# Kernel tuning notes

Measured on AMD Instinct MI355X. Metric: run time of the kernel, lower is better.

## Reference

```python
import jax, jax.numpy as jnp
import numpy as np
import math

N_HEADS = 16
STRIDE = 4
LN_EPS = 1e-5
ROPE_BASE = 10000.0


def rotate_half(x):
    h = x.shape[-1] // 2
    return jnp.concatenate([-x[..., h:], x[..., :h]], axis=-1)


def rope_cos_sin(seq_len, head_dim, dtype):
    inv_freq = 1.0 / (ROPE_BASE ** (jnp.arange(0, head_dim, 2, dtype=jnp.float32) / head_dim))
    t = jnp.arange(seq_len, dtype=jnp.float32)
    freqs = jnp.outer(t, inv_freq)                      # [S, hd/2]
    emb = jnp.concatenate([freqs, freqs], axis=-1)      # [S, hd]
    return jnp.cos(emb).astype(dtype), jnp.sin(emb).astype(dtype)


def linear_upsample(x, T):
    # x: [B, Ts, D] -> [B, T, D]; matches F.interpolate(mode='linear', align_corners=False)
    Ts = x.shape[1]
    scale = Ts / T
    src = (jnp.arange(T, dtype=jnp.float32) + 0.5) * scale - 0.5
    src = jnp.clip(src, 0.0, Ts - 1.0)
    i0 = jnp.floor(src).astype(jnp.int32)
    i1 = jnp.minimum(i0 + 1, Ts - 1)
    w = (src - i0.astype(jnp.float32)).astype(x.dtype)[None, :, None]
    return x[:, i0, :] * (1.0 - w) + x[:, i1, :] * w


def setup_inputs() -> dict:
    key = jax.random.key(0)
    ks = jax.random.split(key, 4)
    B, T, D = 4, 4096, 1024
    s = 1.0 / math.sqrt(D)
    return {
        "x": jax.random.normal(ks[0], (B, T, D), dtype=jnp.float32),
        "norm_w": jnp.ones((D,), dtype=jnp.float32),
        "norm_b": jnp.zeros((D,), dtype=jnp.float32),
        "W_qkv": jax.random.normal(ks[1], (D, 3 * D), dtype=jnp.float32) * s,
        "b_qkv": jnp.zeros((3 * D,), dtype=jnp.float32),
        "W_out": jax.random.normal(ks[2], (D, D), dtype=jnp.float32) * s,
        "b_out": jnp.zeros((D,), dtype=jnp.float32),
    }


def reference(x, norm_w, norm_b, W_qkv, b_qkv, W_out, b_out):
    B, T, D = x.shape
    H = N_HEADS
    hd = D // H
    residual = x

    # LayerNorm (biased variance, eps=1e-5)
    mu = jnp.mean(x, axis=-1, keepdims=True)
    var = jnp.var(x, axis=-1, keepdims=True)
    x_norm = (x - mu) * jax.lax.rsqrt(var + LN_EPS) * norm_w + norm_b

    # strided downsample (T >= 2*stride path)
    xs = x_norm[:, ::STRIDE, :]
    Ts = xs.shape[1]

    # fused QKV projection
    qkv = xs @ W_qkv + b_qkv                             # [B, Ts, 3D]
    qkv = qkv.reshape(B, Ts, 3, H, hd).transpose(2, 0, 3, 1, 4)
    q, k, v = qkv[0], qkv[1], qkv[2]                     # [B, H, Ts, hd]

    # RoPE
    cos, sin = rope_cos_sin(Ts, hd, q.dtype)             # [Ts, hd]
    q = q * cos + rotate_half(q) * sin
    k = k * cos + rotate_half(k) * sin

    # causal SDPA on strided subsequence
    scores = jnp.einsum('bhqd,bhkd->bhqk', q, k) / math.sqrt(hd)
    causal = jnp.tril(jnp.ones((Ts, Ts), dtype=bool))
    scores = jnp.where(causal, scores, jnp.finfo(scores.dtype).min)
    attn = jax.nn.softmax(scores, axis=-1)
    out = jnp.einsum('bhqk,bhkd->bhqd', attn, v)         # [B, H, Ts, hd]
    out = out.transpose(0, 2, 1, 3).reshape(B, Ts, D)

    out = out @ W_out + b_out
    out = linear_upsample(out, T)                        # [B, T, D]
    return residual + out
```

## Files before the change

kernel.cpp:

```cpp
#include <hip/hip_runtime.h>
#include <hip/hip_bf16.h>

#define DEVFN __device__ __forceinline__

typedef float f32x4 __attribute__((ext_vector_type(4)));
typedef float f32x16 __attribute__((ext_vector_type(16)));
typedef __bf16 bf16x8 __attribute__((ext_vector_type(8)));
typedef unsigned short u16x8 __attribute__((ext_vector_type(8)));
typedef unsigned short u16x4 __attribute__((ext_vector_type(4)));
typedef unsigned u32x4 __attribute__((ext_vector_type(4)));

DEVFN unsigned short f2bf(float f) {
  unsigned u = __builtin_bit_cast(unsigned, f);
  u = (u + 0x7FFFu + ((u >> 16) & 1u)) >> 16;
  return (unsigned short)u;
}

DEVFN f32x4 mfma_bf16(u16x8 a, u16x8 b, f32x4 c) {
  return __builtin_amdgcn_mfma_f32_16x16x32_bf16((bf16x8)a, (bf16x8)b, c, 0, 0, 0);
}

DEVFN f32x16 mfma32(u16x8 a, u16x8 b, f32x16 c) {
  return __builtin_amdgcn_mfma_f32_32x32x16_bf16((bf16x8)a, (bf16x8)b, c, 0, 0, 0);
}

DEVFN unsigned cvt_pk_bf16(float a, float b) {
  unsigned r;
  asm("v_cvt_pk_bf16_f32 %0, %1, %2" : "=v"(r) : "v"(a), "v"(b));
  return r;
}

DEVFN void permswap(unsigned& a, unsigned& b) {
  asm("v_permlane32_swap_b32 %0, %1" : "+v"(a), "+v"(b));
}

DEVFN void sincos_rev(float rev, float* sn, float* cs) {
  float fr, s, c;
  asm("v_fract_f32 %0, %1" : "=v"(fr) : "v"(rev));
  asm("v_sin_f32 %0, %1" : "=v"(s) : "v"(fr));
  asm("v_cos_f32 %0, %1" : "=v"(c) : "v"(fr));
  *sn = s; *cs = c;
}

DEVFN void gload_lds16(const void* g, void* l) {
  __builtin_amdgcn_global_load_lds(
      (const __attribute__((address_space(1))) void*)g,
      (__attribute__((address_space(3))) void*)l, 16, 0, 0);
}

__global__ __launch_bounds__(256) void ln_stride_kernel(
    const float* __restrict__ x, const float* __restrict__ w,
    const float* __restrict__ bb, unsigned short* __restrict__ xs,
    int T, int Ts, int D, int stride) {
  int row = blockIdx.x;
  int b = row / Ts, ts = row - b * Ts;
  const float* xr = x + ((size_t)b * T + (size_t)ts * stride) * D;
  int t = threadIdx.x;
  float4 v = *(const float4*)(xr + t * 4);
  float s = v.x + v.y + v.z + v.w;
  float sq = v.x * v.x + v.y * v.y + v.z * v.z + v.w * v.w;
#pragma unroll
  for (int m = 1; m < 64; m <<= 1) { s += __shfl_xor(s, m); sq += __shfl_xor(sq, m); }
  __shared__ float ps[4], pq[4];
  if ((t & 63) == 0) { ps[t >> 6] = s; pq[t >> 6] = sq; }
  __syncthreads();
  s = ps[0] + ps[1] + ps[2] + ps[3];
  sq = pq[0] + pq[1] + pq[2] + pq[3];
  float invD = 1.0f / (float)D;
  float mu = s * invD;
  float var = sq * invD - mu * mu;
  float rs = rsqrtf(var + 1e-5f);
  int c = t * 4;
  float4 wv = *(const float4*)(w + c);
  float4 bv = *(const float4*)(bb + c);
  u16x4 o;
  o[0] = f2bf((v.x - mu) * rs * wv.x + bv.x);
  o[1] = f2bf((v.y - mu) * rs * wv.y + bv.y);
  o[2] = f2bf((v.z - mu) * rs * wv.z + bv.z);
  o[3] = f2bf((v.w - mu) * rs * wv.w + bv.w);
  *(u16x4*)(xs + (size_t)row * D + c) = o;
}

__global__ __launch_bounds__(256) void wconv_kernel(
    const float* __restrict__ W, unsigned short* __restrict__ Wt, int K, int N) {
  __shared__ float tile[32][33];
  int n0 = blockIdx.x * 32, k0 = blockIdx.y * 32;
  int tx = threadIdx.x & 31, ty = threadIdx.x >> 5;
#pragma unroll
  for (int i = 0; i < 32; i += 8) tile[ty + i][tx] = W[(size_t)(k0 + ty + i) * N + n0 + tx];
  __syncthreads();
#pragma unroll
  for (int i = 0; i < 32; i += 8) Wt[(size_t)(n0 + ty + i) * K + k0 + tx] = f2bf(tile[tx][ty + i]);
}

__global__ __launch_bounds__(512, 1) void gemm_qkv256_kernel(
    const unsigned short* __restrict__ A, const unsigned short* __restrict__ Bt,
    const float* __restrict__ bias, int M, int N, int Kd,
    unsigned short* __restrict__ Qo, unsigned short* __restrict__ Ko,
    unsigned short* __restrict__ Vt) {
  __shared__ __align__(128) char lds[131072];
  const int tid = threadIdx.x, l = tid & 63, w = tid >> 6;
  const int wr = w >> 2, wc = w & 3;
  const int lg = l >> 4, lr = l & 15;
  const int o = blockIdx.x;
  const int xcd = o & 7, s = o >> 3;
  const int bm = (xcd & 3) * 4 + (s & 3);
  const int bn = (xcd >> 2) * 6 + (s >> 2);
  const int m0 = bm << 8, n0 = bn << 8;
  const int chk = (lg ^ ((lr >> 1) & 3)) << 4;

  f32x4 acc[8][4] = {};

#define STAGE32(kk, bufoff)                                                 \
  do {                                                                      \
    _Pragma("unroll")                                                       \
    for (int i_ = 0; i_ < 2; i_++) {                                        \
      int c_ = tid + (i_ << 9);                                             \
      int rl_ = c_ >> 2, c4_ = c_ & 3;                                      \
      int cs_ = c4_ ^ ((rl_ >> 1) & 3);                                     \
      gload_lds16(A + (size_t)(m0 + rl_) * Kd + (kk) + cs_ * 8,             \
                  lds + (bufoff) + c_ * 16);                                \
      gload_lds16(Bt + (size_t)(n0 + rl_) * Kd + (kk) + cs_ * 8,            \
                  lds + (bufoff) + 16384 + c_ * 16);                        \
    }                                                                       \
  } while (0)

  STAGE32(0, 0);
  STAGE32(32, 32768);
  STAGE32(64, 65536);

  const int NT = Kd >> 5;
  for (int t = 0; t < NT; ++t) {
    if (t < NT - 2)       asm volatile("s_waitcnt vmcnt(8)" ::: "memory");
    else if (t == NT - 2) asm volatile("s_waitcnt vmcnt(4)" ::: "memory");
    else                  asm volatile("s_waitcnt vmcnt(0)" ::: "memory");
    __builtin_amdgcn_s_barrier();
    const int curoff = (t & 3) << 15;

    u16x8 bfr[4], afr[8];
#pragma unroll
    for (int nf = 0; nf < 4; nf++)
      bfr[nf] = *(const u16x8*)(lds + curoff + 16384 +
                                (wc * 64 + nf * 16 + lr) * 64 + chk);
#pragma unroll
    for (int mf = 0; mf < 8; mf++)
      afr[mf] = *(const u16x8*)(lds + curoff +
                                (wr * 128 + mf * 16 + lr) * 64 + chk);
    if (t + 3 < NT) STAGE32((t + 3) << 5, ((t + 3) & 3) << 15);
    asm volatile("s_waitcnt lgkmcnt(0)" ::: "memory");
    __builtin_amdgcn_sched_barrier(0);
    __builtin_amdgcn_s_setprio(1);
#pragma unroll
    for (int mf = 0; mf < 8; mf++)
#pragma unroll
      for (int nf = 0; nf < 4; nf++)
        acc[mf][nf] = mfma_bf16(afr[mf], bfr[nf], acc[mf][nf]);
    __builtin_amdgcn_s_setprio(0);
    __builtin_amdgcn_s_barrier();
  }
#undef STAGE32

  int nb = n0 + wc * 64;
  int which = nb >> 10;
  int h = (nb & 1023) >> 6;
  if (which < 2) {
    unsigned short* dst = (which == 0) ? Qo : Ko;
    float qsc = (which == 0) ? 0.18033688f : 1.0f;
#pragma unroll
    for (int nt = 0; nt < 2; nt++) {
      int d = nt * 16 + lr;
      float invf_rev = exp2f((float)d * -0.41524101f) * 0.15915494f;
      float blo = bias[nb + nt * 16 + lr];
      float bhi = bias[nb + (nt + 2) * 16 + lr];
#pragma unroll
      for (int mt = 0; mt < 8; mt++) {
        int mb = m0 + wr * 128 + mt * 16 + lg * 4;
#pragma unroll
        for (int r = 0; r < 4; r++) {
          int m = mb + r;
          int b_ = m >> 10, ts = m & 1023;
          float va = acc[mt][nt][r] + blo;
          float vb = acc[mt][nt + 2][r] + bhi;
          float sn, cs;
          sincos_rev((float)ts * invf_rev, &sn, &cs);
          size_t base = (((size_t)(b_ * 16 + h)) * 1024 + ts) * 64;
          dst[base + d] = f2bf((va * cs - vb * sn) * qsc);
          dst[base + d + 32] = f2bf((vb * cs + va * sn) * qsc);
        }
      }
    }
  } else {
#pragma unroll
    for (int nt = 0; nt < 4; nt++) {
      int d = nt * 16 + lr;
      float bi = bias[nb + nt * 16 + lr];
#pragma unroll
      for (int mt = 0; mt < 8; mt++) {
        int mb = m0 + wr * 128 + mt * 16 + lg * 4;
        int b_ = mb >> 10, tsb = mb & 1023;
        u16x4 pk;
#pragma unroll
        for (int r = 0; r < 4; r++) pk[r] = f2bf(acc[mt][nt][r] + bi);
        *(u16x4*)(Vt + (size_t)(b_ * 16 + h) * 65536 +
                  (size_t)(tsb >> 5) * 2048 + d * 32 + (tsb & 31)) = pk;
      }
    }
  }
}

__global__ __launch_bounds__(256) void gemm_out_kernel(
    const unsigned short* __restrict__ A, const unsigned short* __restrict__ Bt,
    const float* __restrict__ bias, int M, int N, int Kd,
    float* __restrict__ Co) {
  __shared__ __align__(128) char lds[49152];
  const int tid = threadIdx.x, l = tid & 63, w = tid >> 6;
  const int wr = w >> 1, wc = w & 1;
  const int lg = l >> 4, lr = l & 15;
  const int o = blockIdx.x;
  const int xcd = o & 7, s = o >> 3;
  const int bm = xcd * 4 + (s & 3);
  const int bn = s >> 2;
  const int m0 = bm << 7, n0 = bn << 7;
  const int chk = (lg ^ ((lr >> 1) & 3)) << 4;

#define STAGE32O(kk, bufoff)                                                \
  do {                                                                      \
    _Pragma("unroll")                                                       \
    for (int i_ = 0; i_ < 2; i_++) {                                        \
      int c_ = tid + (i_ << 8);                                             \
      int rl_ = c_ >> 2, c4_ = c_ & 3;                                      \
      int cs_ = c4_ ^ ((rl_ >> 1) & 3);                                     \
      gload_lds16(A + (size_t)(m0 + rl_) * Kd + (kk) + cs_ * 8,             \
                  lds + (bufoff) + c_ * 16);                                \
      gload_lds16(Bt + (size_t)(n0 + rl_) * Kd + (kk) + cs_ * 8,            \
                  lds + (bufoff) + 8192 + c_ * 16);                         \
    }                                                                       \
  } while (0)

  f32x4 acc[4][4] = {};
  STAGE32O(0, 0);
  STAGE32O(32, 16384);

  const int NT = Kd >> 5;
  for (int t = 0; t < NT; ++t) {
    if (t < NT - 1) asm volatile("s_waitcnt vmcnt(4)" ::: "memory");
    else            asm volatile("s_waitcnt vmcnt(0)" ::: "memory");
    __builtin_amdgcn_s_barrier();
    const int curoff = (t % 3) * 16384;

    u16x8 bfr[4], afr[4];
#pragma unroll
    for (int nf = 0; nf < 4; nf++)
      bfr[nf] = *(const u16x8*)(lds + curoff + 8192 +
                                (wc * 64 + nf * 16 + lr) * 64 + chk);
#pragma unroll
    for (int mf = 0; mf < 4; mf++)
      afr[mf] = *(const u16x8*)(lds + curoff +
                                (wr * 64 + mf * 16 + lr) * 64 + chk);
    if (t + 2 < NT) STAGE32O((t + 2) << 5, ((t + 2) % 3) * 16384);
    asm volatile("s_waitcnt lgkmcnt(0)" ::: "memory");
    __builtin_amdgcn_sched_barrier(0);
    __builtin_amdgcn_s_setprio(1);
#pragma unroll
    for (int mf = 0; mf < 4; mf++)
#pragma unroll
      for (int nf = 0; nf < 4; nf++)
        acc[mf][nf] = mfma_bf16(afr[mf], bfr[nf], acc[mf][nf]);
    __builtin_amdgcn_s_setprio(0);
    __builtin_amdgcn_s_barrier();
  }
#undef STAGE32O

#pragma unroll
  for (int nt = 0; nt < 4; nt++) {
    int n = n0 + wc * 64 + nt * 16 + lr;
    float bi = bias[n];
#pragma unroll
    for (int mt = 0; mt < 4; mt++) {
      int mb = m0 + wr * 64 + mt * 16 + lg * 4;
#pragma unroll
      for (int r = 0; r < 4; r++) Co[(size_t)(mb + r) * N + n] = acc[mt][nt][r] + bi;
    }
  }
}

__global__ __launch_bounds__(256) void attn_kernel(
    const unsigned short* __restrict__ Q, const unsigned short* __restrict__ K,
    const unsigned short* __restrict__ Vt, unsigned short* __restrict__ O,
    int Ts, int H) {
  __shared__ __align__(128) char kvlds[2][16384];
  int t = threadIdx.x, w = t >> 6, l = t & 63;
  int h2 = l >> 5, lq = l & 31;
  int bh = blockIdx.x & 63;
  int i = blockIdx.x >> 6;
  int qg = (i < 4) ? 7 - i : i - 4;
  int b = bh / H, hh = bh % H;
  int qw0 = qg * 128 + w * 32;

  const unsigned short* Qh = Q + ((size_t)bh * Ts) * 64;
  const unsigned short* Kh = K + ((size_t)bh * Ts) * 64;
  const unsigned short* Vh = Vt + (size_t)bh * 65536;

  u16x8 qf[4];
#pragma unroll
  for (int c = 0; c < 4; c++)
    qf[c] = *(const u16x8*)(Qh + (size_t)(qw0 + lq) * 64 + c * 16 + h2 * 8);

#define STAGE_KV(jt, buf)                                                   \
  do {                                                                      \
    _Pragma("unroll")                                                       \
    for (int i_ = 0; i_ < 2; i_++) {                                        \
      int c_ = t + (i_ << 8);                                               \
      int r_ = c_ >> 3, jg_ = c_ & 7;                                       \
      gload_lds16(Kh + (size_t)(jt) * 4096 + r_ * 64 + ((jg_ ^ (r_ & 7)) << 3), \
                  kvlds[buf] + c_ * 16);                                    \
    }                                                                       \
    {                                                                       \
      int d_ = t >> 2, g_ = t & 3;                                          \
      int gs_ = (g_ ^ ((d_ >> 1) & 3)) << 3;                                \
      gload_lds16(Vh + (size_t)(2 * (jt)) * 2048 + d_ * 32 + gs_,           \
                  kvlds[buf] + 8192 + t * 16);                              \
      gload_lds16(Vh + (size_t)(2 * (jt) + 1) * 2048 + d_ * 32 + gs_,       \
                  kvlds[buf] + 12288 + t * 16);                             \
    }                                                                       \
  } while (0)

  f32x16 olo = {}, ohi = {};
  float mrow = -1e30f, lsum = 0.f;
  const int sk = lq & 7;
  const int sv = (lq >> 1) & 3;

  int ntiles = 2 * qg + 2;
  STAGE_KV(0, 0);

  for (int jt = 0; jt < ntiles; jt++) {
    __syncthreads();
    int cur = jt & 1;
    if (jt + 1 < ntiles) STAGE_KV(jt + 1, cur ^ 1);

    int kvt = jt * 64;
    if (kvt > qw0) continue;
    bool haveS1 = (kvt + 32 <= qw0);
    bool diag0 = (kvt == qw0);
    bool diag1 = (kvt + 32 == qw0);

    const char* kb0 = kvlds[cur] + lq * 128;
    const char* kb1 = kvlds[cur] + (32 + lq) * 128;
    u16x8 kf0[4], kf1[4];
#pragma unroll
    for (int c = 0; c < 4; c++)
      kf0[c] = *(const u16x8*)(kb0 + (((c << 1) + h2) ^ sk) * 16);
    f32x16 sA = {}, sB = {};
    if (haveS1) {
#pragma unroll
      for (int c = 0; c < 4; c++)
        kf1[c] = *(const u16x8*)(kb1 + (((c << 1) + h2) ^ sk) * 16);
      __builtin_amdgcn_s_setprio(1);
#pragma unroll
      for (int c = 0; c < 4; c++) sA = mfma32(kf0[c], qf[c], sA);
#pragma unroll
      for (int c = 0; c < 4; c++) sB = mfma32(kf1[c], qf[c], sB);
      __builtin_amdgcn_s_setprio(0);
    } else {
      __builtin_amdgcn_s_setprio(1);
#pragma unroll
      for (int c = 0; c < 4; c++) sA = mfma32(kf0[c], qf[c], sA);
      __builtin_amdgcn_s_setprio(0);
    }

    float p[32];
#pragma unroll
    for (int r = 0; r < 16; r++) {
      float v = sA[r];
      if (diag0) {
        int kvl = (r & 3) + 8 * (r >> 2) + 4 * h2;
        v = (kvl > lq) ? -1e30f : v;
      }
      p[r] = v;
    }
#pragma unroll
    for (int r = 0; r < 16; r++) {
      float v = haveS1 ? sB[r] : -1e30f;
      if (diag1) {
        int kvl = (r & 3) + 8 * (r >> 2) + 4 * h2;
        v = (kvl > lq) ? -1e30f : v;
      }
      p[16 + r] = v;
    }

    float m16[16], m8[8], m4[4];
#pragma unroll
    for (int r = 0; r < 16; r++) m16[r] = fmaxf(p[r], p[16 + r]);
#pragma unroll
    for (int r = 0; r < 8; r++) m8[r] = fmaxf(m16[r], m16[r + 8]);
#pragma unroll
    for (int r = 0; r < 4; r++) m4[r] = fmaxf(m8[r], m8[r + 4]);
    float tmax = fmaxf(fmaxf(m4[0], m4[2]), fmaxf(m4[1], m4[3]));
    tmax = fmaxf(tmax, __shfl_xor(tmax, 32));

    if (!__all(tmax <= mrow + 8.0f)) {
      float mnew = fmaxf(mrow, tmax);
      float al = exp2f(mrow - mnew);
      mrow = mnew;
      lsum *= al;
      olo *= al;
      ohi *= al;
    }

#pragma unroll
    for (int r = 0; r < 32; r++) p[r] = exp2f(p[r] - mrow);
    float s16[16], s8[8], s4[4];
#pragma unroll
    for (int r = 0; r < 16; r++) s16[r] = p[r] + p[16 + r];
#pragma unroll
    for (int r = 0; r < 8; r++) s8[r] = s16[r] + s16[r + 8];
#pragma unroll
    for (int r = 0; r < 4; r++) s4[r] = s8[r] + s8[r + 4];
    lsum += (s4[0] + s4[2]) + (s4[1] + s4[3]);

    {
      unsigned a01 = cvt_pk_bf16(p[0], p[1]),   a23 = cvt_pk_bf16(p[2], p[3]);
      unsigned a45 = cvt_pk_bf16(p[4], p[5]),   a67 = cvt_pk_bf16(p[6], p[7]);
      unsigned a89 = cvt_pk_bf16(p[8], p[9]),   aAB = cvt_pk_bf16(p[10], p[11]);
      unsigned aCD = cvt_pk_bf16(p[12], p[13]), aEF = cvt_pk_bf16(p[14], p[15]);
      permswap(a01, a45);
      permswap(a23, a67);
      permswap(a89, aCD);
      permswap(aAB, aEF);
      u32x4 f0 = {a01, a23, a45, a67};
      u32x4 f1 = {a89, aAB, aCD, aEF};
      u16x8 P0 = __builtin_bit_cast(u16x8, f0);
      u16x8 P1 = __builtin_bit_cast(u16x8, f1);

      const char* vb_ = kvlds[cur] + 8192;
      u16x8 vf[4];
      vf[0] = *(const u16x8*)(vb_ + lq * 64 + ((0 + h2) ^ sv) * 16);
      vf[1] = *(const u16x8*)(vb_ + lq * 64 + ((2 + h2) ^ sv) * 16);
      vf[2] = *(const u16x8*)(vb_ + (32 + lq) * 64 + ((0 + h2) ^ sv) * 16);
      vf[3] = *(const u16x8*)(vb_ + (32 + lq) * 64 + ((2 + h2) ^ sv) * 16);
      __builtin_amdgcn_s_setprio(1);
      olo = mfma32(vf[0], P0, olo);
      olo = mfma32(vf[1], P1, olo);
      ohi = mfma32(vf[2], P0, ohi);
      ohi = mfma32(vf[3], P1, ohi);
      __builtin_amdgcn_s_setprio(0);
    }

    if (haveS1) {
      unsigned b01 = cvt_pk_bf16(p[16], p[17]), b23 = cvt_pk_bf16(p[18], p[19]);
      unsigned b45 = cvt_pk_bf16(p[20], p[21]), b67 = cvt_pk_bf16(p[22], p[23]);
      unsigned b89 = cvt_pk_bf16(p[24], p[25]), bAB = cvt_pk_bf16(p[26], p[27]);
      unsigned bCD = cvt_pk_bf16(p[28], p[29]), bEF = cvt_pk_bf16(p[30], p[31]);
      permswap(b01, b45);
      permswap(b23, b67);
      permswap(b89, bCD);
      permswap(bAB, bEF);
      u32x4 g0 = {b01, b23, b45, b67};
      u32x4 g1 = {b89, bAB, bCD, bEF};
      u16x8 Q0 = __builtin_bit_cast(u16x8, g0);
      u16x8 Q1 = __builtin_bit_cast(u16x8, g1);

      const char* vb_ = kvlds[cur] + 8192 + 4096;
      u16x8 vf[4];
      vf[0] = *(const u16x8*)(vb_ + lq * 64 + ((0 + h2) ^ sv) * 16);
      vf[1] = *(const u16x8*)(vb_ + lq * 64 + ((2 + h2) ^ sv) * 16);
      vf[2] = *(const u16x8*)(vb_ + (32 + lq) * 64 + ((0 + h2) ^ sv) * 16);
      vf[3] = *(const u16x8*)(vb_ + (32 + lq) * 64 + ((2 + h2) ^ sv) * 16);
      __builtin_amdgcn_s_setprio(1);
      olo = mfma32(vf[0], Q0, olo);
      olo = mfma32(vf[1], Q1, olo);
      ohi = mfma32(vf[2], Q0, ohi);
      ohi = mfma32(vf[3], Q1, ohi);
      __builtin_amdgcn_s_setprio(0);
    }
  }
#undef STAGE_KV

  lsum += __shfl_xor(lsum, 32);
  float inv = 1.0f / lsum;
  int q = qw0 + lq;
  unsigned short* orow = O + ((size_t)b * Ts + q) * (size_t)(H * 64) + hh * 64;
#pragma unroll
  for (int g = 0; g < 4; g++) {
    u16x4 plo, phi;
#pragma unroll
    for (int j2 = 0; j2 < 4; j2++) {
      plo[j2] = f2bf(olo[g * 4 + j2] * inv);
      phi[j2] = f2bf(ohi[g * 4 + j2] * inv);
    }
    *(u16x4*)(orow + g * 8 + h2 * 4) = plo;
    *(u16x4*)(orow + 32 + g * 8 + h2 * 4) = phi;
  }
}

__global__ __launch_bounds__(256) void upsample_kernel(
    const float* __restrict__ x, const float* __restrict__ proj,
    float* __restrict__ out, int T, int Ts, int D) {
  int bk = blockIdx.x;
  int b = bk / Ts, k = bk - b * Ts;
  int d4 = threadIdx.x;
  size_t prow = (size_t)b * Ts * D;
  const f32x4 a = *((const f32x4*)(proj + prow + (size_t)max(k - 1, 0) * D) + d4);
  const f32x4 bb = *((const f32x4*)(proj + prow + (size_t)k * D) + d4);
  const f32x4 c = *((const f32x4*)(proj + prow + (size_t)min(k + 1, Ts - 1) * D) + d4);

  size_t xbase = ((size_t)b * T + 4 * (size_t)k) * D + (size_t)d4 * 4;
  f32x4 x0 = __builtin_nontemporal_load((const f32x4*)(x + xbase));
  f32x4 x1 = __builtin_nontemporal_load((const f32x4*)(x + xbase + D));
  f32x4 x2 = __builtin_nontemporal_load((const f32x4*)(x + xbase + 2 * D));
  f32x4 x3 = __builtin_nontemporal_load((const f32x4*)(x + xbase + 3 * D));

  f32x4 o0 = x0 + 0.375f * a + 0.625f * bb;
  f32x4 o1 = x1 + 0.125f * a + 0.875f * bb;
  f32x4 o2 = x2 + 0.875f * bb + 0.125f * c;
  f32x4 o3 = x3 + 0.625f * bb + 0.375f * c;

  __builtin_nontemporal_store(o0, (f32x4*)(out + xbase));
  __builtin_nontemporal_store(o1, (f32x4*)(out + xbase + D));
  __builtin_nontemporal_store(o2, (f32x4*)(out + xbase + 2 * D));
  __builtin_nontemporal_store(o3, (f32x4*)(out + xbase + 3 * D));
}

extern "C" void kernel_launch(void* const* d_in, const int* in_sizes, int n_in,
                              void* d_out, int out_size, void* d_ws, size_t ws_size,
                              hipStream_t stream) {
  (void)in_sizes; (void)n_in; (void)out_size; (void)ws_size;
  const float* x = (const float*)d_in[0];
  const float* norm_w = (const float*)d_in[1];
  const float* norm_b = (const float*)d_in[2];
  const float* W_qkv = (const float*)d_in[3];
  const float* b_qkv = (const float*)d_in[4];
  const float* W_out = (const float*)d_in[5];
  const float* b_out = (const float*)d_in[6];
  float* out = (float*)d_out;

  const int B = 4, T = 4096, D = 1024, H = 16, STR = 4;
  const int Ts = T / STR;
  const int M = B * Ts;

  char* ws = (char*)d_ws;
  unsigned short* xs  = (unsigned short*)(ws);
  unsigned short* Wtq = (unsigned short*)(ws + ((size_t)8 << 20));
  unsigned short* Wto = (unsigned short*)(ws + ((size_t)14 << 20));
  unsigned short* Qb  = (unsigned short*)(ws + ((size_t)16 << 20));
  unsigned short* Kb  = (unsigned short*)(ws + ((size_t)24 << 20));
  unsigned short* Vtb = (unsigned short*)(ws + ((size_t)32 << 20));
  float* proj         = (float*)(ws + ((size_t)16 << 20));
  unsigned short* att = xs;

  ln_stride_kernel<<<M, 256, 0, stream>>>(x, norm_w, norm_b, xs, T, Ts, D, STR);
  wconv_kernel<<<dim3(3 * D / 32, D / 32), 256, 0, stream>>>(W_qkv, Wtq, D, 3 * D);
  wconv_kernel<<<dim3(D / 32, D / 32), 256, 0, stream>>>(W_out, Wto, D, D);
  gemm_qkv256_kernel<<<(M / 256) * (3 * D / 256), 512, 0, stream>>>(
      xs, Wtq, b_qkv, M, 3 * D, D, Qb, Kb, Vtb);
  attn_kernel<<<B * H * 8, 256, 0, stream>>>(Qb, Kb, Vtb, att, Ts, H);
  gemm_out_kernel<<<(M / 128) * (D / 128), 256, 0, stream>>>(
      att, Wto, b_out, M, D, D, proj);
  upsample_kernel<<<B * Ts, 256, 0, stream>>>(x, proj, out, T, Ts, D);
}
```

Baseline: 128.0 us.

## Merge LayerNorm and weight conversions into one prologue; store out-projection in bf16

```diff
diff --git a/kernel.cpp b/kernel.cpp
--- a/kernel.cpp
+++ b/kernel.cpp
@@ -16,6 +16,10 @@
   return (unsigned short)u;
 }
 
+DEVFN float bf2f(unsigned short s) {
+  return __builtin_bit_cast(float, (unsigned)s << 16);
+}
+
 DEVFN f32x4 mfma_bf16(u16x8 a, u16x8 b, f32x4 c) {
   return __builtin_amdgcn_mfma_f32_16x16x32_bf16((bf16x8)a, (bf16x8)b, c, 0, 0, 0);
 }
@@ -48,49 +52,55 @@
       (__attribute__((address_space(3))) void*)l, 16, 0, 0);
 }
 
-__global__ __launch_bounds__(256) void ln_stride_kernel(
+__global__ __launch_bounds__(256) void prologue_kernel(
     const float* __restrict__ x, const float* __restrict__ w,
     const float* __restrict__ bb, unsigned short* __restrict__ xs,
-    int T, int Ts, int D, int stride) {
-  int row = blockIdx.x;
-  int b = row / Ts, ts = row - b * Ts;
-  const float* xr = x + ((size_t)b * T + (size_t)ts * stride) * D;
+    const float* __restrict__ Wq, unsigned short* __restrict__ Wtq,
+    const float* __restrict__ Wo, unsigned short* __restrict__ Wto,
+    int T, int Ts, int D, int stride, int M) {
+  __shared__ float tile[32][33];
+  __shared__ float ps[4], pq[4];
+  int bid = blockIdx.x;
   int t = threadIdx.x;
-  float4 v = *(const float4*)(xr + t * 4);
-  float s = v.x + v.y + v.z + v.w;
-  float sq = v.x * v.x + v.y * v.y + v.z * v.z + v.w * v.w;
-#pragma unroll
-  for (int m = 1; m < 64; m <<= 1) { s += __shfl_xor(s, m); sq += __shfl_xor(sq, m); }
-  __shared__ float ps[4], pq[4];
-  if ((t & 63) == 0) { ps[t >> 6] = s; pq[t >> 6] = sq; }
-  __syncthreads();
-  s = ps[0] + ps[1] + ps[2] + ps[3];
-  sq = pq[0] + pq[1] + pq[2] + pq[3];
-  float invD = 1.0f / (float)D;
-  float mu = s * invD;
-  float var = sq * invD - mu * mu;
-  float rs = rsqrtf(var + 1e-5f);
-  int c = t * 4;
-  float4 wv = *(const float4*)(w + c);
-  float4 bv = *(const float4*)(bb + c);
-  u16x4 o;
-  o[0] = f2bf((v.x - mu) * rs * wv.x + bv.x);
-  o[1] = f2bf((v.y - mu) * rs * wv.y + bv.y);
-  o[2] = f2bf((v.z - mu) * rs * wv.z + bv.z);
-  o[3] = f2bf((v.w - mu) * rs * wv.w + bv.w);
-  *(u16x4*)(xs + (size_t)row * D + c) = o;
-}
-
-__global__ __launch_bounds__(256) void wconv_kernel(
-    const float* __restrict__ W, unsigned short* __restrict__ Wt, int K, int N) {
-  __shared__ float tile[32][33];
-  int n0 = blockIdx.x * 32, k0 = blockIdx.y * 32;
-  int tx = threadIdx.x & 31, ty = threadIdx.x >> 5;
-#pragma unroll
-  for (int i = 0; i < 32; i += 8) tile[ty + i][tx] = W[(size_t)(k0 + ty + i) * N + n0 + tx];
-  __syncthreads();
-#pragma unroll
-  for (int i = 0; i < 32; i += 8) Wt[(size_t)(n0 + ty + i) * K + k0 + tx] = f2bf(tile[tx][ty + i]);
+  if (bid < M) {
+    int b = bid / Ts, ts = bid - b * Ts;
+    const float* xr = x + ((size_t)b * T + (size_t)ts * stride) * D;
+    float4 v = *(const float4*)(xr + t * 4);
+    float s = v.x + v.y + v.z + v.w;
+    float sq = v.x * v.x + v.y * v.y + v.z * v.z + v.w * v.w;
+#pragma unroll
+    for (int m = 1; m < 64; m <<= 1) { s += __shfl_xor(s, m); sq += __shfl_xor(sq, m); }
+    if ((t & 63) == 0) { ps[t >> 6] = s; pq[t >> 6] = sq; }
+    __syncthreads();
+    s = ps[0] + ps[1] + ps[2] + ps[3];
+    sq = pq[0] + pq[1] + pq[2] + pq[3];
+    float invD = 1.0f / (float)D;
+    float mu = s * invD;
+    float var = sq * invD - mu * mu;
+    float rs = rsqrtf(var + 1e-5f);
+    int c = t * 4;
+    float4 wv = *(const float4*)(w + c);
+    float4 bv = *(const float4*)(bb + c);
+    u16x4 o;
+    o[0] = f2bf((v.x - mu) * rs * wv.x + bv.x);
+    o[1] = f2bf((v.y - mu) * rs * wv.y + bv.y);
+    o[2] = f2bf((v.z - mu) * rs * wv.z + bv.z);
+    o[3] = f2bf((v.w - mu) * rs * wv.w + bv.w);
+    *(u16x4*)(xs + (size_t)bid * D + c) = o;
+  } else {
+    const float* W; unsigned short* Wt; int N, b2;
+    b2 = bid - M;
+    if (b2 < (3 * D / 32) * (D / 32)) { W = Wq; Wt = Wtq; N = 3 * D; }
+    else { b2 -= (3 * D / 32) * (D / 32); W = Wo; Wt = Wto; N = D; }
+    int nb = N / 32;
+    int n0 = (b2 % nb) * 32, k0 = (b2 / nb) * 32;
+    int tx = t & 31, ty = t >> 5;
+#pragma unroll
+    for (int i = 0; i < 32; i += 8) tile[ty + i][tx] = W[(size_t)(k0 + ty + i) * N + n0 + tx];
+    __syncthreads();
+#pragma unroll
+    for (int i = 0; i < 32; i += 8) Wt[(size_t)(n0 + ty + i) * D + k0 + tx] = f2bf(tile[tx][ty + i]);
+  }
 }
 
 __global__ __launch_bounds__(512, 1) void gemm_qkv256_kernel(
@@ -211,7 +221,7 @@
 __global__ __launch_bounds__(256) void gemm_out_kernel(
     const unsigned short* __restrict__ A, const unsigned short* __restrict__ Bt,
     const float* __restrict__ bias, int M, int N, int Kd,
-    float* __restrict__ Co) {
+    unsigned short* __restrict__ Co) {
   __shared__ __align__(128) char lds[49152];
   const int tid = threadIdx.x, l = tid & 63, w = tid >> 6;
   const int wr = w >> 1, wc = w & 1;
@@ -279,7 +289,8 @@
     for (int mt = 0; mt < 4; mt++) {
       int mb = m0 + wr * 64 + mt * 16 + lg * 4;
 #pragma unroll
-      for (int r = 0; r < 4; r++) Co[(size_t)(mb + r) * N + n] = acc[mt][nt][r] + bi;
+      for (int r = 0; r < 4; r++)
+        Co[(size_t)(mb + r) * N + n] = f2bf(acc[mt][nt][r] + bi);
     }
   }
 }
@@ -494,15 +505,20 @@
 }
 
 __global__ __launch_bounds__(256) void upsample_kernel(
-    const float* __restrict__ x, const float* __restrict__ proj,
+    const float* __restrict__ x, const unsigned short* __restrict__ proj,
     float* __restrict__ out, int T, int Ts, int D) {
   int bk = blockIdx.x;
   int b = bk / Ts, k = bk - b * Ts;
   int d4 = threadIdx.x;
   size_t prow = (size_t)b * Ts * D;
-  const f32x4 a = *((const f32x4*)(proj + prow + (size_t)max(k - 1, 0) * D) + d4);
-  const f32x4 bb = *((const f32x4*)(proj + prow + (size_t)k * D) + d4);
-  const f32x4 c = *((const f32x4*)(proj + prow + (size_t)min(k + 1, Ts - 1) * D) + d4);
+  u16x4 av = *((const u16x4*)(proj + prow + (size_t)max(k - 1, 0) * D) + d4);
+  u16x4 bv = *((const u16x4*)(proj + prow + (size_t)k * D) + d4);
+  u16x4 cv = *((const u16x4*)(proj + prow + (size_t)min(k + 1, Ts - 1) * D) + d4);
+  f32x4 a, bb, c;
+#pragma unroll
+  for (int j = 0; j < 4; j++) {
+    a[j] = bf2f(av[j]); bb[j] = bf2f(bv[j]); c[j] = bf2f(cv[j]);
+  }
 
   size_t xbase = ((size_t)b * T + 4 * (size_t)k) * D + (size_t)d4 * 4;
   f32x4 x0 = __builtin_nontemporal_load((const f32x4*)(x + xbase));
@@ -545,12 +561,11 @@
   unsigned short* Qb  = (unsigned short*)(ws + ((size_t)16 << 20));
   unsigned short* Kb  = (unsigned short*)(ws + ((size_t)24 << 20));
   unsigned short* Vtb = (unsigned short*)(ws + ((size_t)32 << 20));
-  float* proj         = (float*)(ws + ((size_t)16 << 20));
+  unsigned short* proj = (unsigned short*)(ws + ((size_t)16 << 20));
   unsigned short* att = xs;
 
-  ln_stride_kernel<<<M, 256, 0, stream>>>(x, norm_w, norm_b, xs, T, Ts, D, STR);
-  wconv_kernel<<<dim3(3 * D / 32, D / 32), 256, 0, stream>>>(W_qkv, Wtq, D, 3 * D);
-  wconv_kernel<<<dim3(D / 32, D / 32), 256, 0, stream>>>(W_out, Wto, D, D);
+  prologue_kernel<<<M + (3 * D / 32) * (D / 32) + (D / 32) * (D / 32), 256, 0, stream>>>(
+      x, norm_w, norm_b, xs, W_qkv, Wtq, W_out, Wto, T, Ts, D, STR, M);
   gemm_qkv256_kernel<<<(M / 256) * (3 * D / 256), 512, 0, stream>>>(
       xs, Wtq, b_qkv, M, 3 * D, D, Qb, Kb, Vtb);
   attn_kernel<<<B * H * 8, 256, 0, stream>>>(Qb, Kb, Vtb, att, Ts, H);
```

Result: faster. 118.4 us (median of 2 runs) (-7.5%).
